# Optimization experiments

Hardware: AMD Instinct MI355X
Metric: run time of the kernel (lower is better)

## Reference

```python
import jax, jax.numpy as jnp
import numpy as np

DX = 0.01
DT = 0.5
MU_UP = 0.001

_lap = np.array([[0,0,-1/12,0,0],[0,0,4/3,0,0],[-1/12,4/3,-5,4/3,-1/12],[0,0,4/3,0,0],[0,0,-1/12,0,0]], dtype=np.float32)
_dx = np.array([[0,0,1/12,0,0],[0,0,-8/12,0,0],[0,0,0,0,0],[0,0,8/12,0,0],[0,0,-1/12,0,0]], dtype=np.float32)
K_LAP = jnp.asarray(_lap)[None, None] / (DX * DX)   # [1,1,5,5]
K_DX = jnp.asarray(_dx)[None, None] / DX             # derivative along H axis (torch res_dx)
K_DY = jnp.swapaxes(K_DX, 2, 3)                      # derivative along W axis (torch res_dy)


def _conv(x, k):
    # cross-correlation, VALID, NCHW -- matches torch Conv2d
    return jax.lax.conv_general_dilated(x, k, (1, 1), 'VALID',
                                        dimension_numbers=('NCHW', 'OIHW', 'NCHW'))


def _pad(h):
    # periodic padding of 2 on both spatial dims (torch.cat based circular pad)
    return jnp.pad(h, ((0, 0), (0, 0), (2, 2), (2, 2)), mode='wrap')


def _f_rhs(u, v, Re, UA, UB, VA, VB):
    up, vp = _pad(u), _pad(v)
    u_x, u_y = _conv(up, K_DX), _conv(up, K_DY)
    v_x, v_y = _conv(vp, K_DX), _conv(vp, K_DY)
    nu = MU_UP / Re
    f_u = nu * _conv(up, K_LAP) + UA * u * u_x + UB * v * u_y
    f_v = nu * _conv(vp, K_LAP) + VA * u * v_x + VB * v * v_y
    return f_u, f_v


def setup_inputs() -> dict:
    key = jax.random.key(0)
    k_h, k_re, k_ua, k_ub, k_va, k_vb = jax.random.split(key, 6)
    h = jax.random.normal(k_h, (8, 2, 1024, 1024), dtype=jnp.float32)
    Re = jax.random.uniform(k_re, (), jnp.float32, 0.5, 1.5)  # keep 1/Re well-conditioned
    UA = jax.random.uniform(k_ua, (), jnp.float32)
    UB = jax.random.uniform(k_ub, (), jnp.float32)
    VA = jax.random.uniform(k_va, (), jnp.float32)
    VB = jax.random.uniform(k_vb, (), jnp.float32)
    return {'h': h, 'Re': Re, 'UA': UA, 'UB': UB, 'VA': VA, 'VB': VB}


def reference(h, Re, UA, UB, VA, VB):
    u0 = h[:, 0:1]
    v0 = h[:, 1:2]
    k1u, k1v = _f_rhs(u0, v0, Re, UA, UB, VA, VB)
    k2u, k2v = _f_rhs(u0 + k1u * (DT / 2.0), v0 + k1v * (DT / 2.0), Re, UA, UB, VA, VB)
    k3u, k3v = _f_rhs(u0 + k2u * (DT / 2.0), v0 + k2v * (DT / 2.0), Re, UA, UB, VA, VB)
    k4u, k4v = _f_rhs(u0 + k3u * DT, v0 + k3v * DT, Re, UA, UB, VA, VB)
    u_next = u0 + DT * (k1u + 2 * k2u + 2 * k3u + k4u) / 6.0
    v_next = v0 + DT * (k1v + 2 * k2v + 2 * k3v + k4v) / 6.0
    return jnp.concatenate((u_next, v_next), axis=1)
```

## Files before the change

kernel.cpp:

```cpp
#include <hip/hip_runtime.h>


typedef float f4 __attribute__((ext_vector_type(4)));
typedef float f2 __attribute__((ext_vector_type(2)));

#define LCOLS 88
#define LROWS 84
#define NBUF  (LROWS*LCOLS)
#define NT    1024
#define NQ    2

__global__ __launch_bounds__(NT, 4)
void rk4_stencil(const float* __restrict__ h,
                 const float* __restrict__ sRe, const float* __restrict__ sUA,
                 const float* __restrict__ sUB, const float* __restrict__ sVA,
                 const float* __restrict__ sVB, float* __restrict__ out)
{
    __shared__ __align__(16) float tu[NBUF];
    __shared__ __align__(16) float tv[NBUF];

    const int tid = threadIdx.x;
    const int tc = blockIdx.x, tr = blockIdx.y, bb = blockIdx.z;

    const float Re = sRe[0], UA = sUA[0], UB = sUB[0], VA = sVA[0], VB = sVB[0];
    const float nu = 0.001f / Re;

    const float d1 = 800.f/12.f;
    const float d2 = 100.f/12.f;
    const float a1 = (4.f/3.f)*1.0e4f;
    const float a2 = -(1.f/12.f)*1.0e4f;
    const float a0 = -5.0e4f;

    const f4 z4 = {0.f, 0.f, 0.f, 0.f};

    {
        int i = tid;
        if (i < 320) {
            int row = 2 + (i % 80);
            int rest = i / 80;
            float* p = ((rest >> 1) ? tv : tu) + row*LCOLS + ((rest & 1) ? 84 : 0);
            *(f4*)p = z4;
        }
    }

    const size_t plane = 1048576;
    const float* uin = h + (size_t)(bb*2) * plane;
    const float* vin = uin + plane;
    const int base_r = tr*64 - 8, base_c = tc*64 - 8;

#pragma unroll
    for (int m = 0; m < 2; ++m) {
        int g = tid + NT*m;
        if (g < 1600) {
            int r = g / 20, k = g - r*20;
            int gr = (base_r + r) & 1023;
            int gc = (base_c + 4*k) & 1023;
            int l = (r+2)*LCOLS + 4 + 4*k;
            *(f4*)(tu + l) = *(const f4*)(uin + (size_t)gr*1024 + gc);
            *(f4*)(tv + l) = *(const f4*)(vin + (size_t)gr*1024 + gc);
        }
    }
    __syncthreads();

    int  lidx[NQ]; bool has[NQ]; int qrA[NQ], qcA[NQ];
    f4 ku[NQ], kv[NQ], au[NQ], av[NQ];
#pragma unroll
    for (int j = 0; j < NQ; ++j) {
        int q = tid + NT*j;
        has[j] = (q < 1600);
        int qr = q / 20, qc = q - qr*20;
        qrA[j] = qr; qcA[j] = qc;
        lidx[j] = (qr+2)*LCOLS + 4 + 4*qc;
        ku[j] = z4; kv[j] = z4; au[j] = z4; av[j] = z4;
    }

    const int rowlo[4] = {2, 4, 6, 8};
    const int rowhi[4] = {78, 76, 74, 72};
    const int qclo[4]  = {0, 1, 1, 2};
    const int qchi[4]  = {20, 19, 19, 18};
    const float csub_t[4] = {0.f, 0.25f, 0.25f, 0.5f};
    const float cadd_t[4] = {0.25f, 0.25f, 0.5f, 0.f};
    const float wgt_t[4]  = {1.f, 2.f, 2.f, 1.f};

    float* outu = out + (size_t)(bb*2) * plane;
    float* outv = outu + plane;

#pragma unroll
    for (int s = 0; s < 4; ++s) {
        const float wgt  = wgt_t[s];
        const float csub = csub_t[s];
        const float cadd = cadd_t[s];
        f4 stu[NQ], stv[NQ];
        bool act[NQ];
#pragma unroll
        for (int j = 0; j < NQ; ++j) {
            act[j] = has[j] && qrA[j] >= rowlo[s] && qrA[j] < rowhi[s]
                            && qcA[j] >= qclo[s]  && qcA[j] < qchi[s];
            if (!act[j]) continue;
            const int l = lidx[j];
            f4 ucc = *(const f4*)(tu+l);
            f2 ul2 = *(const f2*)(tu+l-2);
            f2 ur2 = *(const f2*)(tu+l+4);
            f4 un1 = *(const f4*)(tu+l-LCOLS);
            f4 us1 = *(const f4*)(tu+l+LCOLS);
            f4 un2 = *(const f4*)(tu+l-2*LCOLS);
            f4 us2 = *(const f4*)(tu+l+2*LCOLS);
            f4 vcc = *(const f4*)(tv+l);
            f2 vl2 = *(const f2*)(tv+l-2);
            f2 vr2 = *(const f2*)(tv+l+4);
            f4 vn1 = *(const f4*)(tv+l-LCOLS);
            f4 vs1 = *(const f4*)(tv+l+LCOLS);
            f4 vn2 = *(const f4*)(tv+l-2*LCOLS);
            f4 vs2 = *(const f4*)(tv+l+2*LCOLS);
            float hu[8] = {ul2[0],ul2[1],ucc[0],ucc[1],ucc[2],ucc[3],ur2[0],ur2[1]};
            float hv[8] = {vl2[0],vl2[1],vcc[0],vcc[1],vcc[2],vcc[3],vr2[0],vr2[1]};
            f4 ou, ov;
#pragma unroll
            for (int k = 0; k < 4; ++k) {
                float u = hu[k+2], v = hv[k+2];
                float urow = d1*(us1[k]-un1[k]) + d2*(un2[k]-us2[k]);
                float vrow = d1*(vs1[k]-vn1[k]) + d2*(vn2[k]-vs2[k]);
                float ucol = d1*(hu[k+3]-hu[k+1]) + d2*(hu[k]-hu[k+4]);
                float vcol = d1*(hv[k+3]-hv[k+1]) + d2*(hv[k]-hv[k+4]);
                float ulap = a1*((un1[k]+us1[k])+(hu[k+1]+hu[k+3]))
                           + a2*((un2[k]+us2[k])+(hu[k]+hu[k+4])) + a0*u;
                float vlap = a1*((vn1[k]+vs1[k])+(hv[k+1]+hv[k+3]))
                           + a2*((vn2[k]+vs2[k])+(hv[k]+hv[k+4])) + a0*v;
                float fu = nu*ulap + UA*(u*urow) + UB*(v*ucol);
                float fv = nu*vlap + VA*(u*vrow) + VB*(v*vcol);
                float kuold = ku[j][k], kvold = kv[j][k];
                if (s == 3) {
                    ou[k] = (u - 0.5f*kuold) + (1.f/12.f)*(au[j][k] + fu);
                    ov[k] = (v - 0.5f*kvold) + (1.f/12.f)*(av[j][k] + fv);
                } else {
                    au[j][k] += wgt*fu;
                    av[j][k] += wgt*fv;
                    stu[j][k] = (u - csub*kuold) + cadd*fu;
                    stv[j][k] = (v - csub*kvold) + cadd*fv;
                    ku[j][k] = fu;
                    kv[j][k] = fv;
                }
            }
            if (s == 3) {
                int gr = tr*64 + qrA[j] - 8;
                int gc = tc*64 + 4*qcA[j] - 8;
                __builtin_nontemporal_store(ou, (f4*)(outu + (size_t)gr*1024 + gc));
                __builtin_nontemporal_store(ov, (f4*)(outv + (size_t)gr*1024 + gc));
            }
        }
        if (s < 3) {
            __syncthreads();
#pragma unroll
            for (int j = 0; j < NQ; ++j) {
                if (!act[j]) continue;
                *(f4*)(tu+lidx[j]) = stu[j];
                *(f4*)(tv+lidx[j]) = stv[j];
            }
            __syncthreads();
        }
    }
}

extern "C" void kernel_launch(void* const* d_in, const int* in_sizes, int n_in,
                              void* d_out, int out_size, void* d_ws, size_t ws_size,
                              hipStream_t stream) {
    const float* h   = (const float*)d_in[0];
    const float* sRe = (const float*)d_in[1];
    const float* sUA = (const float*)d_in[2];
    const float* sUB = (const float*)d_in[3];
    const float* sVA = (const float*)d_in[4];
    const float* sVB = (const float*)d_in[5];
    float* o = (float*)d_out;
    rk4_stencil<<<dim3(16,16,8), dim3(NT,1,1), 0, stream>>>(h, sRe, sUA, sUB, sVA, sVB, o);
}
```

Before: 208.9 us.

## Load halo tile directly into LDS with global_load_lds and widen tile row pitch

Replaces the register-staged global-to-shared tile copy with direct global-to-LDS loads (global_load_lds, 16 bytes per lane), reshaping the shared tile to 80x96 so each wave fills contiguous 256-float chunks. Column offsets shift by 8 so the loaded halo covers the stencil without the separate zeroing pass. Launch bounds raise the occupancy hint to 8. The goal is to cut VGPR traffic and instruction count in the load phase. The cost is extra halo columns fetched from memory and tighter register pressure from the higher occupancy hint.

```diff
diff --git a/kernel.cpp b/kernel.cpp
--- a/kernel.cpp
+++ b/kernel.cpp
@@ -4,13 +4,17 @@
 typedef float f4 __attribute__((ext_vector_type(4)));
 typedef float f2 __attribute__((ext_vector_type(2)));
 
-#define LCOLS 88
-#define LROWS 84
+#define LCOLS 96
+#define LROWS 80
 #define NBUF  (LROWS*LCOLS)
 #define NT    1024
 #define NQ    2
 
-__global__ __launch_bounds__(NT, 4)
+#define GLOAD16(gp, lp) __builtin_amdgcn_global_load_lds(                      \
+    (const __attribute__((address_space(1))) void*)(gp),                       \
+    (__attribute__((address_space(3))) void*)(lp), 16, 0, 0)
+
+__global__ __launch_bounds__(NT, 8)
 void rk4_stencil(const float* __restrict__ h,
                  const float* __restrict__ sRe, const float* __restrict__ sUA,
                  const float* __restrict__ sUB, const float* __restrict__ sVA,
@@ -33,31 +37,29 @@
 
     const f4 z4 = {0.f, 0.f, 0.f, 0.f};
 
-    {
-        int i = tid;
-        if (i < 320) {
-            int row = 2 + (i % 80);
-            int rest = i / 80;
-            float* p = ((rest >> 1) ? tv : tu) + row*LCOLS + ((rest & 1) ? 84 : 0);
-            *(f4*)p = z4;
-        }
-    }
-
     const size_t plane = 1048576;
     const float* uin = h + (size_t)(bb*2) * plane;
     const float* vin = uin + plane;
-    const int base_r = tr*64 - 8, base_c = tc*64 - 8;
+    const int base_r = tr*64 - 8  + 1024;
+    const int base_c = tc*64 - 16 + 1024;
 
+    {
+        const int wave = tid >> 6, lane = tid & 63;
 #pragma unroll
-    for (int m = 0; m < 2; ++m) {
-        int g = tid + NT*m;
-        if (g < 1600) {
-            int r = g / 20, k = g - r*20;
-            int gr = (base_r + r) & 1023;
-            int gc = (base_c + 4*k) & 1023;
-            int l = (r+2)*LCOLS + 4 + 4*k;
-            *(f4*)(tu + l) = *(const f4*)(uin + (size_t)gr*1024 + gc);
-            *(f4*)(tv + l) = *(const f4*)(vin + (size_t)gr*1024 + gc);
+        for (int it = 0; it < 4; ++it) {
+            int c = wave + 16*it;
+            if (c < 60) {
+                int fld = (c >= 30);
+                int cc  = fld ? (c - 30) : c;
+                int idx = 256*cc + 4*lane;
+                int row = idx / LCOLS;
+                int col = idx - row*LCOLS;
+                int gr = (base_r + row) & 1023;
+                int gc = (base_c + col) & 1023;
+                const float* gp = (fld ? vin : uin) + ((size_t)gr << 10) + gc;
+                float* lp = (fld ? tv : tu) + 256*cc;
+                GLOAD16(gp, lp);
+            }
         }
     }
     __syncthreads();
@@ -67,17 +69,17 @@
 #pragma unroll
     for (int j = 0; j < NQ; ++j) {
         int q = tid + NT*j;
-        has[j] = (q < 1600);
-        int qr = q / 20, qc = q - qr*20;
+        has[j] = (j == 0) || (q < 1600);
+        int qr = q / 20, qc = q - qr*20 + 2;
         qrA[j] = qr; qcA[j] = qc;
-        lidx[j] = (qr+2)*LCOLS + 4 + 4*qc;
+        lidx[j] = qr*LCOLS + 4*qc;
         ku[j] = z4; kv[j] = z4; au[j] = z4; av[j] = z4;
     }
 
     const int rowlo[4] = {2, 4, 6, 8};
     const int rowhi[4] = {78, 76, 74, 72};
-    const int qclo[4]  = {0, 1, 1, 2};
-    const int qchi[4]  = {20, 19, 19, 18};
+    const int qclo[4]  = {2, 3, 3, 4};
+    const int qchi[4]  = {22, 21, 21, 20};
     const float csub_t[4] = {0.f, 0.25f, 0.25f, 0.5f};
     const float cadd_t[4] = {0.25f, 0.25f, 0.5f, 0.f};
     const float wgt_t[4]  = {1.f, 2.f, 2.f, 1.f};
@@ -143,7 +145,7 @@
             }
             if (s == 3) {
                 int gr = tr*64 + qrA[j] - 8;
-                int gc = tc*64 + 4*qcA[j] - 8;
+                int gc = tc*64 + 4*qcA[j] - 16;
                 __builtin_nontemporal_store(ou, (f4*)(outu + (size_t)gr*1024 + gc));
                 __builtin_nontemporal_store(ov, (f4*)(outv + (size_t)gr*1024 + gc));
             }
```

Result: slower. 546.4 us (+161.5%).
